# Kernel optimization log

Hardware: AMD Instinct MI355X
Metric: run time of the kernel (lower is better)

The kernel has to match this reference:

```python
import jax, jax.numpy as jnp
import numpy as np

HEADS = 4
REDUCTION = 4
BN_EPS = 1e-5


def conv1x1_bn(x, W, b, gamma, beta, mean, var):
    # x: [B, C, W, H]; 1x1 conv == channel matmul, then BN (inference form)
    y = jnp.einsum('oc,bcwh->bowh', W, x) + b[None, :, None, None]
    scale = (gamma / jnp.sqrt(var + BN_EPS))[None, :, None, None]
    return (y - mean[None, :, None, None]) * scale + beta[None, :, None, None]


def setup_inputs() -> dict:
    key = jax.random.key(0)
    ks = jax.random.split(key, 24)
    C, Cq = 512, 512 // REDUCTION  # 128
    B, Wd, Hd = 16, 32, 32
    dh = Cq // HEADS  # 32
    rnd = lambda k, s: jax.random.normal(k, s, dtype=jnp.float32)
    pos = lambda k, s: jax.random.uniform(k, s, dtype=jnp.float32, minval=0.5, maxval=1.5)
    return {
        'x': rnd(ks[0], (B, C, Wd, Hd)),
        'Wq': rnd(ks[1], (Cq, C)) * 0.05, 'bq': rnd(ks[2], (Cq,)) * 0.05,
        'q_gamma': pos(ks[3], (Cq,)), 'q_beta': rnd(ks[4], (Cq,)) * 0.05,
        'q_mean': rnd(ks[5], (Cq,)) * 0.05, 'q_var': pos(ks[6], (Cq,)),
        'Wk': rnd(ks[7], (Cq, C)) * 0.05, 'bk': rnd(ks[8], (Cq,)) * 0.05,
        'k_gamma': pos(ks[9], (Cq,)), 'k_beta': rnd(ks[10], (Cq,)) * 0.05,
        'k_mean': rnd(ks[11], (Cq,)) * 0.05, 'k_var': pos(ks[12], (Cq,)),
        'Wv': rnd(ks[13], (C, C)) * 0.05, 'bv': rnd(ks[14], (C,)) * 0.05,
        'v_gamma': pos(ks[15], (C,)), 'v_beta': rnd(ks[16], (C,)) * 0.05,
        'v_mean': rnd(ks[17], (C,)) * 0.05, 'v_var': pos(ks[18], (C,)),
        'rel_h': rnd(ks[19], (1, HEADS, dh, 1, Hd)),
        'rel_w': rnd(ks[20], (1, HEADS, dh, Wd, 1)),
    }


def reference(x, Wq, bq, q_gamma, q_beta, q_mean, q_var,
              Wk, bk, k_gamma, k_beta, k_mean, k_var,
              Wv, bv, v_gamma, v_beta, v_mean, v_var,
              rel_h, rel_w):
    B, C, Wd, Hd = x.shape
    N = Wd * Hd
    dh = C // REDUCTION // HEADS
    dv = C // HEADS
    q = conv1x1_bn(x, Wq, bq, q_gamma, q_beta, q_mean, q_var).reshape(B, HEADS, dh, N)
    k = conv1x1_bn(x, Wk, bk, k_gamma, k_beta, k_mean, k_var).reshape(B, HEADS, dh, N)
    v = conv1x1_bn(x, Wv, bv, v_gamma, v_beta, v_mean, v_var).reshape(B, HEADS, dv, N)
    # content-content: q^T k -> [B, H, N, N]
    cc = jnp.einsum('bhdn,bhdm->bhnm', q, k)
    # content-position: (rel_h + rel_w) flattened to [H, dh, N], then pos^T @ q
    pos = (rel_h + rel_w).reshape(HEADS, dh, N)
    cp = jnp.einsum('hdn,bhdm->bhnm', pos, q)
    attn = jax.nn.softmax(cc + cp, axis=-1)
    # out = v @ attn^T  (torch: matmul(v, attention.permute(0,1,3,2)))
    out = jnp.einsum('bhcn,bhmn->bhcm', v, attn)
    return out.reshape(B, C, Wd, Hd) + x
```

## Files before the change

kernel.cpp:

```cpp
#include <hip/hip_runtime.h>


typedef _Float16 f16x8 __attribute__((ext_vector_type(8)));
typedef __attribute__((ext_vector_type(4))) float f32x4;
typedef __attribute__((ext_vector_type(4))) unsigned int u32x4;
typedef __attribute__((ext_vector_type(2))) unsigned int u32x2;

#define MFMAH(a, b, c) __builtin_amdgcn_mfma_f32_16x16x32_f16(a, b, c, 0, 0, 0)
#define LOG2E 1.4426950408889634f

__device__ __forceinline__ unsigned pkh(float a, float b) {
  auto p = __builtin_amdgcn_cvt_pkrtz(a, b);
  return __builtin_bit_cast(unsigned, p);
}
__device__ __forceinline__ short f2h(float a) {
  _Float16 h = (_Float16)a;
  return __builtin_bit_cast(short, h);
}

__device__ __forceinline__ void gload16(const void* g, void* l) {
  __builtin_amdgcn_global_load_lds(
      (const __attribute__((address_space(1))) void*)g,
      (__attribute__((address_space(3))) void*)l, 16, 0, 0);
}

__global__ __launch_bounds__(256) void setup_kernel(
    const float* __restrict__ Wq, const float* __restrict__ bq,
    const float* __restrict__ qg, const float* __restrict__ qbe,
    const float* __restrict__ qme, const float* __restrict__ qva,
    const float* __restrict__ Wk, const float* __restrict__ bk,
    const float* __restrict__ kg, const float* __restrict__ kbe,
    const float* __restrict__ kme, const float* __restrict__ kva,
    const float* __restrict__ Wv, const float* __restrict__ bv,
    const float* __restrict__ vg, const float* __restrict__ vbe,
    const float* __restrict__ vme, const float* __restrict__ vva,
    const float* __restrict__ rel_h, const float* __restrict__ rel_w,
    unsigned short* __restrict__ Wh, float* __restrict__ bfv,
    unsigned short* __restrict__ posH)
{
  int bid = blockIdx.x;
  if (bid < 1536) {
    int idx = bid * 256 + threadIdx.x;
    if (idx >= 768 * 512) return;
    int o = idx >> 9, c = idx & 511;
    float w, sc, bb, mean, beta, post;
    if (o < 128) {
      sc = qg[o] / sqrtf(qva[o] + 1e-5f);
      w = Wq[o * 512 + c]; bb = bq[o]; mean = qme[o]; beta = qbe[o];
      post = LOG2E;
    } else if (o < 256) {
      int r = o - 128;
      sc = kg[r] / sqrtf(kva[r] + 1e-5f);
      w = Wk[r * 512 + c]; bb = bk[r]; mean = kme[r]; beta = kbe[r];
      post = 1.0f;
    } else {
      int r = o - 256;
      sc = vg[r] / sqrtf(vva[r] + 1e-5f);
      w = Wv[r * 512 + c]; bb = bv[r]; mean = vme[r]; beta = vbe[r];
      post = 1.0f;
    }
    Wh[idx] = (unsigned short)f2h(w * sc * post);
    if (c == 0) bfv[o] = ((bb - mean) * sc + beta) * post;
  } else {
    int idx = (bid - 1536) * 256 + threadIdx.x;
    if (idx >= 4 * 1024 * 32) return;
    int h = idx >> 15, rem = idx & 32767, n = rem >> 5, d = rem & 31;
    int w = n >> 5, hh = n & 31;
    float v = rel_h[(h * 32 + d) * 32 + hh] + rel_w[(h * 32 + d) * 32 + w];
    posH[idx] = (unsigned short)f2h(v);
  }
}

__global__ __launch_bounds__(512) void proj_kernel(
    const float* __restrict__ x,
    const unsigned short* __restrict__ Wh, const float* __restrict__ bfv,
    unsigned short* __restrict__ qH, unsigned short* __restrict__ kH,
    unsigned short* __restrict__ vH)
{
  __shared__ __align__(16) short sm[16384];

  int bid = blockIdx.x;
  int b = bid / 48, rem = bid % 48, mblk = rem >> 3, nblk = rem & 7;
  int Mb = mblk * 128, Nb = nblk * 128;
  int t = threadIdx.x;
  int lane = t & 63, w = t >> 6, ln = lane & 15, g = (lane >> 4) & 3;
  int wm = w >> 2, wn = w & 3;
  int kg8 = t >> 6, np = t & 63;
  int n0 = 2 * np;
  int swp = (np >> 2) & 1;

  f32x4 acc[4][2];
  for (int i = 0; i < 4; i++)
    for (int j = 0; j < 2; j++) acc[i][j] = (f32x4){0.f, 0.f, 0.f, 0.f};

  for (int kb = 0; kb < 512; kb += 64) {
    __syncthreads();
    for (int i = 0; i < 2; i++) {
      int grp = w + i * 8;
      int unit = grp * 64 + lane;
      int row = unit >> 3, pos = unit & 7;
      int j = pos ^ (row & 7);
      gload16(&Wh[(Mb + row) * 512 + kb + j * 8], &sm[grp * 512]);
    }
    {
      float2 fB[8];
      for (int rr = 0; rr < 8; rr++)
        fB[rr] = *(const float2*)&x[(b * 512 + kb + kg8 * 8 + rr) * 1024 +
                                    Nb + n0];
      short* Bt = sm + 8192;
      u32x4 wE = (u32x4){pkh(fB[0].x, fB[1].x), pkh(fB[2].x, fB[3].x),
                         pkh(fB[4].x, fB[5].x), pkh(fB[6].x, fB[7].x)};
      u32x4 wO = (u32x4){pkh(fB[0].y, fB[1].y), pkh(fB[2].y, fB[3].y),
                         pkh(fB[4].y, fB[5].y), pkh(fB[6].y, fB[7].y)};
      int offE = n0 * 64 + 8 * (kg8 ^ (n0 & 7));
      int offO = (n0 + 1) * 64 + 8 * (kg8 ^ ((n0 + 1) & 7));
      int o1 = swp ? offO : offE, o2 = swp ? offE : offO;
      u32x4 d1 = swp ? wO : wE, d2 = swp ? wE : wO;
      *(u32x4*)&Bt[o1] = d1;
      *(u32x4*)&Bt[o2] = d2;
    }
    __syncthreads();

    const short* Bt = sm + 8192;
    for (int ks = 0; ks < 2; ks++) {
      f16x8 af[4], bf[2];
      for (int mt = 0; mt < 4; mt++) {
        int o = wm * 64 + mt * 16 + ln;
        af[mt] = *(const f16x8*)&sm[o * 64 + 8 * ((ks * 4 + g) ^ (o & 7))];
      }
      for (int nt = 0; nt < 2; nt++) {
        int n = wn * 32 + nt * 16 + ln;
        bf[nt] = *(const f16x8*)&Bt[n * 64 + 8 * ((ks * 4 + g) ^ (n & 7))];
      }
      __builtin_amdgcn_s_setprio(1);
      for (int mt = 0; mt < 4; mt++)
        for (int nt = 0; nt < 2; nt++)
          acc[mt][nt] = MFMAH(af[mt], bf[nt], acc[mt][nt]);
      __builtin_amdgcn_s_setprio(0);
    }
  }

  unsigned* smU = (unsigned*)sm;
  for (int p = 0; p < 2; p++) {
    __syncthreads();
    if ((wn >> 1) == p) {
      if (mblk < 2) {
        for (int mt = 0; mt < 4; mt++)
          for (int nt = 0; nt < 2; nt++) {
            float y0 = acc[mt][nt][0] + bfv[Mb + wm * 64 + mt * 16 + g * 4 + 0];
            float y1 = acc[mt][nt][1] + bfv[Mb + wm * 64 + mt * 16 + g * 4 + 1];
            float y2 = acc[mt][nt][2] + bfv[Mb + wm * 64 + mt * 16 + g * 4 + 2];
            float y3 = acc[mt][nt][3] + bfv[Mb + wm * 64 + mt * 16 + g * 4 + 3];
            u32x2 pk = (u32x2){pkh(y0, y1), pkh(y2, y3)};
            int nl = (wn & 1) * 32 + nt * 16 + ln;
            *(u32x2*)&smU[nl * 66 + wm * 32 + mt * 8 + g * 2] = pk;
          }
      } else {
        for (int mt = 0; mt < 4; mt++)
          for (int nt = 0; nt < 2; nt++)
            for (int r = 0; r < 4; r++) {
              int o = wm * 64 + mt * 16 + g * 4 + r;
              sm[o * 72 + (wn & 1) * 32 + nt * 16 + ln] =
                  f2h(acc[mt][nt][r] + bfv[Mb + o]);
            }
      }
    }
    __syncthreads();
    if (mblk < 2) {
      unsigned short* dh = (mblk == 0) ? qH : kH;
      for (int it = 0; it < 2; it++) {
        int task = it * 512 + t;
        int h = task >> 8, nl = (task >> 2) & 63, qc = task & 3;
        u32x4 v4 = *(const u32x4*)&smU[nl * 66 + h * 16 + qc * 4];
        int gi = ((b * 4 + h) * 1024 + Nb + p * 64 + nl) * 32 + qc * 8;
        *(u32x4*)&dh[gi] = v4;
      }
    } else {
      int bh = b * 4 + (mblk - 2);
      for (int it = 0; it < 2; it++) {
        int task = it * 512 + t;
        int o = task >> 3, qc = task & 7;
        u32x4 vv = *(const u32x4*)&sm[o * 72 + qc * 8];
        *(u32x4*)&vH[(bh * 128 + o) * 1024 + Nb + p * 64 + qc * 8] = vv;
      }
    }
  }
}

__global__ __launch_bounds__(512, 4) void attn_kernel(
    const float* __restrict__ x,
    const unsigned short* __restrict__ qH, const unsigned short* __restrict__ kH,
    const unsigned short* __restrict__ posH, const unsigned short* __restrict__ vH,
    float* __restrict__ out)
{
  __shared__ __align__(16) short sm[2 * 12288 + 8 * 1152];

  int bid = blockIdx.x;
  int bh = (bid & 7) * 8 + ((bid >> 3) & 7);
  int qt = bid >> 6;
  int b = bh >> 2, h = bh & 3;
  int t = threadIdx.x;
  int lane = t & 63, w = t >> 6, ln = lane & 15, g = (lane >> 4) & 3;

  int qrow = qt * 128 + w * 16 + ln;
  f16x8 bQ   = *(const f16x8*)&qH[(bh * 1024 + qrow) * 32 + g * 8];
  f16x8 bPos = *(const f16x8*)&posH[(h * 1024 + qrow) * 32 + g * 8];

  f16x8 aOnes;
  {
    _Float16 o1 = (ln == 0) ? (_Float16)1.0f : (_Float16)0.0f;
    for (int i = 0; i < 8; i++) aOnes[i] = o1;
  }

  f32x4 acc[9];
  for (int ct = 0; ct < 9; ct++) acc[ct] = (f32x4){0.f, 0.f, 0.f, 0.f};
  float m_run = -1e30f;

  short* Pw = &sm[24576 + w * 1152];

  auto STAGE = [&](int bb, int jb) {
    {
      int u = t & 255;
      int r = u >> 2;
      int ch = (u & 3) ^ (r & 3) ^ ((r >> 2) & 3);
      long gq = (long)(bh * 1024 + jb + r) * 32 + ch * 8;
      const unsigned short* src = (t < 256) ? kH : qH;
      short* base = &sm[bb * 12288 + ((t < 256) ? 0 : 2048) + (w & 3) * 512];
      gload16(&src[gq], base);
    }
    for (int i = 0; i < 2; i++) {
      int u = t + i * 512;
      int c = u >> 3;
      int vch = (u & 7) ^ (c & 7);
      long gv = (long)(bh * 128 + c) * 1024 + jb + vch * 8;
      short* base = &sm[bb * 12288 + 4096 + (w + i * 8) * 512];
      gload16(&vH[gv], base);
    }
  };

  STAGE(0, 0);

  for (int it = 0; it < 16; ++it) {
    int cur = it & 1;
    if (it < 15) {
      STAGE(cur ^ 1, (it + 1) * 64);
      asm volatile("s_waitcnt vmcnt(3)" ::: "memory");
    } else {
      asm volatile("s_waitcnt vmcnt(0)" ::: "memory");
    }
    __builtin_amdgcn_s_barrier();
    __builtin_amdgcn_sched_barrier(0);

    const short* B = &sm[cur * 12288];

    f16x8 aK[4], aQ[4];
    for (int kt = 0; kt < 4; kt++) {
      int r = kt * 16 + ln;
      int p = g ^ (r & 3) ^ ((r >> 2) & 3);
      int off = r * 32 + p * 8;
      aK[kt] = *(const f16x8*)&B[off];
      aQ[kt] = *(const f16x8*)&B[2048 + off];
    }

    f32x4 s[4];
    for (int kt = 0; kt < 4; kt++) s[kt] = (f32x4){0.f, 0.f, 0.f, 0.f};
    __builtin_amdgcn_s_setprio(1);
    for (int kt = 0; kt < 4; kt++) s[kt] = MFMAH(aK[kt], bQ, s[kt]);
    for (int kt = 0; kt < 4; kt++) s[kt] = MFMAH(aQ[kt], bPos, s[kt]);
    __builtin_amdgcn_s_setprio(0);

    float m0 = fmaxf(fmaxf(s[0][0], s[0][1]), fmaxf(s[0][2], s[0][3]));
    float m1 = fmaxf(fmaxf(s[1][0], s[1][1]), fmaxf(s[1][2], s[1][3]));
    float m2 = fmaxf(fmaxf(s[2][0], s[2][1]), fmaxf(s[2][2], s[2][3]));
    float m3 = fmaxf(fmaxf(s[3][0], s[3][1]), fmaxf(s[3][2], s[3][3]));
    float mx = fmaxf(fmaxf(m0, m1), fmaxf(m2, m3));
    if (__any(mx > m_run + 8.f)) {
      float mxf = fmaxf(mx, __shfl_xor(mx, 16));
      mxf = fmaxf(mxf, __shfl_xor(mxf, 32));
      float mnew = fmaxf(m_run, mxf);
      float scl = __builtin_amdgcn_exp2f(m_run - mnew);
      for (int ct = 0; ct < 9; ct++) acc[ct] *= scl;
      m_run = mnew;
    }
    for (int kt = 0; kt < 4; kt++)
      for (int r = 0; r < 4; r++)
        s[kt][r] = __builtin_amdgcn_exp2f(s[kt][r] - m_run);

    for (int kt = 0; kt < 4; kt++) {
      u32x2 pk = (u32x2){pkh(s[kt][0], s[kt][1]), pkh(s[kt][2], s[kt][3])};
      *(u32x2*)&Pw[ln * 72 + kt * 16 + g * 4] = pk;
    }
    asm volatile("s_waitcnt lgkmcnt(0)" ::: "memory");
    __builtin_amdgcn_sched_barrier(0);
    f16x8 pFrag[2];
    for (int st2 = 0; st2 < 2; st2++)
      pFrag[st2] = *(const f16x8*)&Pw[ln * 72 + st2 * 32 + g * 8];

    __builtin_amdgcn_s_setprio(1);
    acc[8] = MFMAH(aOnes, pFrag[0], acc[8]);
    acc[8] = MFMAH(aOnes, pFrag[1], acc[8]);
    for (int ct = 0; ct < 8; ct++)
      for (int st2 = 0; st2 < 2; st2++) {
        int c = ct * 16 + ln;
        int pos = (st2 * 4 + g) ^ (c & 7);
        f16x8 av = *(const f16x8*)&B[4096 + c * 64 + pos * 8];
        acc[ct] = MFMAH(av, pFrag[st2], acc[ct]);
      }
    __builtin_amdgcn_s_setprio(0);

    __builtin_amdgcn_sched_barrier(0);
    __builtin_amdgcn_s_barrier();
    __builtin_amdgcn_sched_barrier(0);
  }

  float lsum = __shfl(acc[8][0], ln);
  float inv = 1.0f / lsum;
  int m = qt * 128 + w * 16 + ln;
  for (int ct = 0; ct < 8; ct++)
    for (int r = 0; r < 4; r++) {
      int c = h * 128 + ct * 16 + g * 4 + r;
      int gi = (b * 512 + c) * 1024 + m;
      out[gi] = acc[ct][r] * inv + x[gi];
    }
}

extern "C" void kernel_launch(void* const* d_in, const int* in_sizes, int n_in,
                              void* d_out, int out_size, void* d_ws, size_t ws_size,
                              hipStream_t stream) {
  const float* x    = (const float*)d_in[0];
  const float* Wq   = (const float*)d_in[1];
  const float* bq   = (const float*)d_in[2];
  const float* qg   = (const float*)d_in[3];
  const float* qbe  = (const float*)d_in[4];
  const float* qme  = (const float*)d_in[5];
  const float* qva  = (const float*)d_in[6];
  const float* Wk   = (const float*)d_in[7];
  const float* bk   = (const float*)d_in[8];
  const float* kg   = (const float*)d_in[9];
  const float* kbe  = (const float*)d_in[10];
  const float* kme  = (const float*)d_in[11];
  const float* kva  = (const float*)d_in[12];
  const float* Wv   = (const float*)d_in[13];
  const float* bv   = (const float*)d_in[14];
  const float* vg   = (const float*)d_in[15];
  const float* vbe  = (const float*)d_in[16];
  const float* vme  = (const float*)d_in[17];
  const float* vva  = (const float*)d_in[18];
  const float* relh = (const float*)d_in[19];
  const float* relw = (const float*)d_in[20];
  float* outp = (float*)d_out;

  unsigned char* ws = (unsigned char*)d_ws;
  unsigned short* Whp  = (unsigned short*)(ws + 0);
  float*          bfv  = (float*)(ws + 786432);
  unsigned short* qHp  = (unsigned short*)(ws + 789504);
  unsigned short* kHp  = (unsigned short*)(ws + 4983808);
  unsigned short* posHp= (unsigned short*)(ws + 9178112);
  unsigned short* vHp  = (unsigned short*)(ws + 9440256);

  setup_kernel<<<2048, 256, 0, stream>>>(Wq, bq, qg, qbe, qme, qva,
                                         Wk, bk, kg, kbe, kme, kva,
                                         Wv, bv, vg, vbe, vme, vva,
                                         relh, relw, Whp, bfv, posHp);
  proj_kernel<<<768, 512, 0, stream>>>(x, Whp, bfv, qHp, kHp, vHp);
  attn_kernel<<<512, 512, 0, stream>>>(x, qHp, kHp, posHp, vHp, outp);
}
```

Baseline: 76.72 us.

## Process two query sub-tiles per wave to reuse staged K/Q/V tiles

Each attention block now handles 256 query rows instead of 128. Every wave keeps two query fragments, two softmax running maxima and two accumulator sets. Each V fragment read from LDS feeds two MFMAs, which halves LDS staging and global K/V traffic per query row. The grid drops from 512 to 256 blocks and occupancy bounds fall from 4 to 2, so there is less parallelism to hide latency and more register pressure.

```diff
diff --git a/kernel.cpp b/kernel.cpp
--- a/kernel.cpp
+++ b/kernel.cpp
@@ -187,13 +187,13 @@
   }
 }
 
-__global__ __launch_bounds__(512, 4) void attn_kernel(
+__global__ __launch_bounds__(512, 2) void attn_kernel(
     const float* __restrict__ x,
     const unsigned short* __restrict__ qH, const unsigned short* __restrict__ kH,
     const unsigned short* __restrict__ posH, const unsigned short* __restrict__ vH,
     float* __restrict__ out)
 {
-  __shared__ __align__(16) short sm[2 * 12288 + 8 * 1152];
+  __shared__ __align__(16) short sm[2 * 12288 + 8 * 2304];
 
   int bid = blockIdx.x;
   int bh = (bid & 7) * 8 + ((bid >> 3) & 7);
@@ -202,9 +202,13 @@
   int t = threadIdx.x;
   int lane = t & 63, w = t >> 6, ln = lane & 15, g = (lane >> 4) & 3;
 
-  int qrow = qt * 128 + w * 16 + ln;
-  f16x8 bQ   = *(const f16x8*)&qH[(bh * 1024 + qrow) * 32 + g * 8];
-  f16x8 bPos = *(const f16x8*)&posH[(h * 1024 + qrow) * 32 + g * 8];
+  f16x8 bQ[2], bPos[2];
+#pragma unroll
+  for (int qs = 0; qs < 2; qs++) {
+    int qrow = qt * 256 + qs * 128 + w * 16 + ln;
+    bQ[qs]   = *(const f16x8*)&qH[(bh * 1024 + qrow) * 32 + g * 8];
+    bPos[qs] = *(const f16x8*)&posH[(h * 1024 + qrow) * 32 + g * 8];
+  }
 
   f16x8 aOnes;
   {
@@ -212,11 +216,13 @@
     for (int i = 0; i < 8; i++) aOnes[i] = o1;
   }
 
-  f32x4 acc[9];
-  for (int ct = 0; ct < 9; ct++) acc[ct] = (f32x4){0.f, 0.f, 0.f, 0.f};
-  float m_run = -1e30f;
-
-  short* Pw = &sm[24576 + w * 1152];
+  f32x4 acc[2][9];
+#pragma unroll
+  for (int qs = 0; qs < 2; qs++)
+    for (int ct = 0; ct < 9; ct++) acc[qs][ct] = (f32x4){0.f, 0.f, 0.f, 0.f};
+  float m_run[2] = {-1e30f, -1e30f};
+
+  short* Pw = &sm[24576 + w * 2304];
 
   auto STAGE = [&](int bb, int jb) {
     {
@@ -262,50 +268,59 @@
       aQ[kt] = *(const f16x8*)&B[2048 + off];
     }
 
-    f32x4 s[4];
-    for (int kt = 0; kt < 4; kt++) s[kt] = (f32x4){0.f, 0.f, 0.f, 0.f};
-    __builtin_amdgcn_s_setprio(1);
-    for (int kt = 0; kt < 4; kt++) s[kt] = MFMAH(aK[kt], bQ, s[kt]);
-    for (int kt = 0; kt < 4; kt++) s[kt] = MFMAH(aQ[kt], bPos, s[kt]);
-    __builtin_amdgcn_s_setprio(0);
-
-    float m0 = fmaxf(fmaxf(s[0][0], s[0][1]), fmaxf(s[0][2], s[0][3]));
-    float m1 = fmaxf(fmaxf(s[1][0], s[1][1]), fmaxf(s[1][2], s[1][3]));
-    float m2 = fmaxf(fmaxf(s[2][0], s[2][1]), fmaxf(s[2][2], s[2][3]));
-    float m3 = fmaxf(fmaxf(s[3][0], s[3][1]), fmaxf(s[3][2], s[3][3]));
-    float mx = fmaxf(fmaxf(m0, m1), fmaxf(m2, m3));
-    if (__any(mx > m_run + 8.f)) {
-      float mxf = fmaxf(mx, __shfl_xor(mx, 16));
-      mxf = fmaxf(mxf, __shfl_xor(mxf, 32));
-      float mnew = fmaxf(m_run, mxf);
-      float scl = __builtin_amdgcn_exp2f(m_run - mnew);
-      for (int ct = 0; ct < 9; ct++) acc[ct] *= scl;
-      m_run = mnew;
-    }
-    for (int kt = 0; kt < 4; kt++)
-      for (int r = 0; r < 4; r++)
-        s[kt][r] = __builtin_amdgcn_exp2f(s[kt][r] - m_run);
-
-    for (int kt = 0; kt < 4; kt++) {
-      u32x2 pk = (u32x2){pkh(s[kt][0], s[kt][1]), pkh(s[kt][2], s[kt][3])};
-      *(u32x2*)&Pw[ln * 72 + kt * 16 + g * 4] = pk;
+#pragma unroll
+    for (int qs = 0; qs < 2; qs++) {
+      f32x4 s[4];
+      for (int kt = 0; kt < 4; kt++) s[kt] = (f32x4){0.f, 0.f, 0.f, 0.f};
+      __builtin_amdgcn_s_setprio(1);
+      for (int kt = 0; kt < 4; kt++) s[kt] = MFMAH(aK[kt], bQ[qs], s[kt]);
+      for (int kt = 0; kt < 4; kt++) s[kt] = MFMAH(aQ[kt], bPos[qs], s[kt]);
+      __builtin_amdgcn_s_setprio(0);
+
+      float m0 = fmaxf(fmaxf(s[0][0], s[0][1]), fmaxf(s[0][2], s[0][3]));
+      float m1 = fmaxf(fmaxf(s[1][0], s[1][1]), fmaxf(s[1][2], s[1][3]));
+      float m2 = fmaxf(fmaxf(s[2][0], s[2][1]), fmaxf(s[2][2], s[2][3]));
+      float m3 = fmaxf(fmaxf(s[3][0], s[3][1]), fmaxf(s[3][2], s[3][3]));
+      float mx = fmaxf(fmaxf(m0, m1), fmaxf(m2, m3));
+      if (__any(mx > m_run[qs] + 8.f)) {
+        float mxf = fmaxf(mx, __shfl_xor(mx, 16));
+        mxf = fmaxf(mxf, __shfl_xor(mxf, 32));
+        float mnew = fmaxf(m_run[qs], mxf);
+        float scl = __builtin_amdgcn_exp2f(m_run[qs] - mnew);
+        for (int ct = 0; ct < 9; ct++) acc[qs][ct] *= scl;
+        m_run[qs] = mnew;
+      }
+      for (int kt = 0; kt < 4; kt++)
+        for (int r = 0; r < 4; r++)
+          s[kt][r] = __builtin_amdgcn_exp2f(s[kt][r] - m_run[qs]);
+
+      for (int kt = 0; kt < 4; kt++) {
+        u32x2 pk = (u32x2){pkh(s[kt][0], s[kt][1]), pkh(s[kt][2], s[kt][3])};
+        *(u32x2*)&Pw[qs * 1152 + ln * 72 + kt * 16 + g * 4] = pk;
+      }
     }
     asm volatile("s_waitcnt lgkmcnt(0)" ::: "memory");
     __builtin_amdgcn_sched_barrier(0);
-    f16x8 pFrag[2];
-    for (int st2 = 0; st2 < 2; st2++)
-      pFrag[st2] = *(const f16x8*)&Pw[ln * 72 + st2 * 32 + g * 8];
+    f16x8 pFrag[2][2];
+#pragma unroll
+    for (int qs = 0; qs < 2; qs++)
+      for (int st2 = 0; st2 < 2; st2++)
+        pFrag[qs][st2] =
+            *(const f16x8*)&Pw[qs * 1152 + ln * 72 + st2 * 32 + g * 8];
 
     __builtin_amdgcn_s_setprio(1);
-    acc[8] = MFMAH(aOnes, pFrag[0], acc[8]);
-    acc[8] = MFMAH(aOnes, pFrag[1], acc[8]);
     for (int ct = 0; ct < 8; ct++)
       for (int st2 = 0; st2 < 2; st2++) {
         int c = ct * 16 + ln;
         int pos = (st2 * 4 + g) ^ (c & 7);
         f16x8 av = *(const f16x8*)&B[4096 + c * 64 + pos * 8];
-        acc[ct] = MFMAH(av, pFrag[st2], acc[ct]);
-      }
+        acc[0][ct] = MFMAH(av, pFrag[0][st2], acc[0][ct]);
+        acc[1][ct] = MFMAH(av, pFrag[1][st2], acc[1][ct]);
+      }
+    acc[0][8] = MFMAH(aOnes, pFrag[0][0], acc[0][8]);
+    acc[0][8] = MFMAH(aOnes, pFrag[0][1], acc[0][8]);
+    acc[1][8] = MFMAH(aOnes, pFrag[1][0], acc[1][8]);
+    acc[1][8] = MFMAH(aOnes, pFrag[1][1], acc[1][8]);
     __builtin_amdgcn_s_setprio(0);
 
     __builtin_amdgcn_sched_barrier(0);
@@ -313,15 +328,18 @@
     __builtin_amdgcn_sched_barrier(0);
   }
 
-  float lsum = __shfl(acc[8][0], ln);
-  float inv = 1.0f / lsum;
-  int m = qt * 128 + w * 16 + ln;
-  for (int ct = 0; ct < 8; ct++)
-    for (int r = 0; r < 4; r++) {
-      int c = h * 128 + ct * 16 + g * 4 + r;
-      int gi = (b * 512 + c) * 1024 + m;
-      out[gi] = acc[ct][r] * inv + x[gi];
-    }
+#pragma unroll
+  for (int qs = 0; qs < 2; qs++) {
+    float lsum = __shfl(acc[qs][8][0], ln);
+    float inv = 1.0f / lsum;
+    int m = qt * 256 + qs * 128 + w * 16 + ln;
+    for (int ct = 0; ct < 8; ct++)
+      for (int r = 0; r < 4; r++) {
+        int c = h * 128 + ct * 16 + g * 4 + r;
+        int gi = (b * 512 + c) * 1024 + m;
+        out[gi] = acc[qs][ct][r] * inv + x[gi];
+      }
+  }
 }
 
 extern "C" void kernel_launch(void* const* d_in, const int* in_sizes, int n_in,
@@ -363,5 +381,5 @@
                                          Wv, bv, vg, vbe, vme, vva,
                                          relh, relw, Whp, bfv, posHp);
   proj_kernel<<<768, 512, 0, stream>>>(x, Whp, bfv, qHp, kHp, vHp);
-  attn_kernel<<<512, 512, 0, stream>>>(x, qHp, kHp, posHp, vHp, outp);
-}
+  attn_kernel<<<256, 512, 0, stream>>>(x, qHp, kHp, posHp, vHp, outp);
+}
```

Result: no change. 76.67 us (-0.1%).
